# Kernel optimization log

Hardware: AMD Instinct MI355X
Metric: run time of the kernel (lower is better)

The kernel has to match this reference:

```python
import jax, jax.numpy as jnp
import numpy as np

HIDDEN = 1024
HEADS = 16
HEAD_DIM = HIDDEN // HEADS

def setup_inputs() -> dict:
    key = jax.random.key(0)
    k1, k2, k3 = jax.random.split(key, 3)
    scale = 1.0 / np.sqrt(HIDDEN)
    return {
        "x": jax.random.normal(k1, (2, 2048, HIDDEN), dtype=jnp.float32),
        "w_qkv": jax.random.normal(k2, (HIDDEN, 3 * HIDDEN), dtype=jnp.float32) * scale,
        "b_qkv": jnp.zeros((3 * HIDDEN,), dtype=jnp.float32),
        "w_out": jax.random.normal(k3, (HIDDEN, HIDDEN), dtype=jnp.float32) * scale,
        "b_out": jnp.zeros((HIDDEN,), dtype=jnp.float32),
    }

def reference(x, w_qkv, b_qkv, w_out, b_out):
    B, S, H = x.shape
    qkv = x @ w_qkv + b_qkv                              # (B,S,3H)
    qkv = qkv.reshape(B, S, 3, HEADS, HEAD_DIM)
    qkv = jnp.transpose(qkv, (2, 0, 3, 1, 4))            # (3,B,nh,S,hd)
    q, k, v = qkv[0], qkv[1], qkv[2]
    scores = jnp.einsum("bhqd,bhkd->bhqk", q, k) / np.sqrt(HEAD_DIM)
    causal = jnp.triu(jnp.ones((S, S), dtype=bool), k=1)  # True above diagonal
    scores = jnp.where(causal, -jnp.inf, scores)
    attn = jax.nn.softmax(scores, axis=-1)               # dropout: eval mode (identity)
    out = jnp.einsum("bhqk,bhkd->bhqd", attn, v)
    out = jnp.transpose(out, (0, 2, 1, 3)).reshape(B, S, H)
    return out @ w_out + b_out
```

## Files before the change

kernel.cpp:

```cpp
#include <hip/hip_runtime.h>
#include <hip/hip_bf16.h>

typedef short short8 __attribute__((ext_vector_type(8)));
typedef float f32x4 __attribute__((ext_vector_type(4)));

typedef const __attribute__((address_space(1))) unsigned int* gas_ptr;
typedef __attribute__((address_space(3))) unsigned int* las_ptr;
#define ASYNC16(g, l) __builtin_amdgcn_global_load_lds((gas_ptr)(g), (las_ptr)(l), 16, 0, 0)

__device__ __forceinline__ unsigned short f2bf(float f) {
    unsigned int u = __builtin_bit_cast(unsigned int, f);
    u += 0x7fff + ((u >> 16) & 1);
    return (unsigned short)(u >> 16);
}
__device__ __forceinline__ float bf2f(unsigned short s) {
    unsigned int u = (unsigned int)s << 16;
    return __builtin_bit_cast(float, u);
}
__device__ __forceinline__ unsigned int pkbf_trunc(float lo, float hi) {
    return __builtin_amdgcn_perm(__builtin_bit_cast(unsigned int, hi),
                                 __builtin_bit_cast(unsigned int, lo), 0x07060302u);
}
__device__ __forceinline__ float fexp2(float x) {
#if __has_builtin(__builtin_amdgcn_exp2f)
    return __builtin_amdgcn_exp2f(x);
#else
    return __expf(x * 0.6931471805599453f);
#endif
}

__device__ __forceinline__ void transpose_tile(
    const float* __restrict__ w, unsigned short* __restrict__ wt,
    int K, int N, int k0, int n0, unsigned short* tile)
{
    for (int i = threadIdx.x; i < 64 * 64; i += 256) {
        int r = i >> 6, c = i & 63;
        tile[r * 65 + c] = f2bf(w[(size_t)(k0 + r) * N + n0 + c]);
    }
    __syncthreads();
    for (int i = threadIdx.x; i < 64 * 64; i += 256) {
        int r = i >> 6, c = i & 63;
        wt[(size_t)(n0 + r) * K + k0 + c] = tile[c * 65 + r];
    }
}

__global__ __launch_bounds__(256) void prep(
    const float* __restrict__ x, const float* __restrict__ w_qkv,
    const float* __restrict__ w_out,
    unsigned short* __restrict__ x_b, unsigned short* __restrict__ wqkv_t,
    unsigned short* __restrict__ wout_t)
{
    __shared__ unsigned short tile[64 * 65];
    int bid = blockIdx.x;
    if (bid < 4096) {
        int i = (bid * 256 + threadIdx.x) * 4;
        float4 v = *(const float4*)(x + i);
        ushort4 o;
        o.x = f2bf(v.x); o.y = f2bf(v.y); o.z = f2bf(v.z); o.w = f2bf(v.w);
        *(ushort4*)(x_b + i) = o;
    } else if (bid < 4096 + 768) {
        int t = bid - 4096;
        transpose_tile(w_qkv, wqkv_t, 1024, 3072, (t / 48) * 64, (t % 48) * 64, tile);
    } else {
        int t = bid - 4864;
        transpose_tile(w_out, wout_t, 1024, 1024, (t >> 4) * 64, (t & 15) * 64, tile);
    }
}


template<bool OUT_BF16, bool QKV>
__global__ __launch_bounds__(256, 3) void gemm_bt(
    const unsigned short* __restrict__ A,
    const unsigned short* __restrict__ Bt,
    const float* __restrict__ bias,
    void* __restrict__ C,
    unsigned short* __restrict__ vTp,
    int M, int N, int K)
{
    __shared__ __align__(16) unsigned short As[2][128 * 32];
    __shared__ __align__(16) unsigned short Bs[2][128 * 32];
    const int tid = threadIdx.x;
    const int lane = tid & 63;
    const int wave = tid >> 6;
    const int wr = wave >> 1, wc = wave & 1;
    const int m0 = blockIdx.x * 128, n0 = blockIdx.y * 128;
    const int fr = lane & 15, fq = lane >> 4;

    f32x4 acc[4][4] = {};

    const int grow = lane >> 2;
    const int gcol = (lane & 3) * 8;
    const unsigned short* Ag = A  + (size_t)(m0 + wave * 32 + grow) * K + gcol;
    const unsigned short* Bg = Bt + (size_t)(n0 + wave * 32 + grow) * K + gcol;
    const int wb0 = (wave * 32) * 32;
    const int wb1 = (wave * 32 + 16) * 32;

    for (int k0 = 0; k0 < K; k0 += 64) {
        __syncthreads();
        ASYNC16(Ag + k0,               As[0] + wb0);
        ASYNC16(Ag + 16 * K + k0,      As[0] + wb1);
        ASYNC16(Bg + k0,               Bs[0] + wb0);
        ASYNC16(Bg + 16 * K + k0,      Bs[0] + wb1);
        ASYNC16(Ag + k0 + 32,          As[1] + wb0);
        ASYNC16(Ag + 16 * K + k0 + 32, As[1] + wb1);
        ASYNC16(Bg + k0 + 32,          Bs[1] + wb0);
        ASYNC16(Bg + 16 * K + k0 + 32, Bs[1] + wb1);
        __syncthreads();

#pragma unroll
        for (int h = 0; h < 2; h++) {
            short8 af[4], bfr[4];
#pragma unroll
            for (int i = 0; i < 4; i++)
                af[i] = *(const short8*)(As[h] + (wr * 64 + i * 16 + fr) * 32 + fq * 8);
#pragma unroll
            for (int j = 0; j < 4; j++)
                bfr[j] = *(const short8*)(Bs[h] + (wc * 64 + j * 16 + fr) * 32 + fq * 8);
#pragma unroll
            for (int i = 0; i < 4; i++)
#pragma unroll
                for (int j = 0; j < 4; j++)
                    acc[i][j] = __builtin_amdgcn_mfma_f32_16x16x32_bf16(af[i], bfr[j], acc[i][j], 0, 0, 0);
        }
    }

#pragma unroll
    for (int i = 0; i < 4; i++)
#pragma unroll
        for (int j = 0; j < 4; j++) {
            int col = n0 + wc * 64 + j * 16 + fr;
            float bv = bias[col];
            if (QKV && col >= 2048) {
                int hh = (col - 2048) >> 6, d = col & 63;
#pragma unroll
                for (int r = 0; r < 4; r++) {
                    int row = m0 + wr * 64 + i * 16 + fq * 4 + r;
                    int bb = row >> 11, s = row & 2047;
                    vTp[((size_t)(bb * 16 + hh) * 64 + d) * 2048 + s] = f2bf(acc[i][j][r] + bv);
                }
            } else {
                const int cstride = QKV ? 2048 : N;
#pragma unroll
                for (int r = 0; r < 4; r++) {
                    int row = m0 + wr * 64 + i * 16 + fq * 4 + r;
                    float v = acc[i][j][r] + bv;
                    if (OUT_BF16)
                        ((unsigned short*)C)[(size_t)row * cstride + col] = f2bf(v);
                    else
                        ((float*)C)[(size_t)row * cstride + col] = v;
                }
            }
        }
}


template<int RG0>
__device__ __forceinline__ void attn_step(
    const unsigned short* __restrict__ Ks0, const unsigned short* __restrict__ Ks1,
    const unsigned short* __restrict__ Vs0, const unsigned short* __restrict__ Vs1,
    unsigned short* __restrict__ Psw,
    const short8 (&qf)[4][2], const short8 ones,
    f32x4 (&o_acc)[4][4], f32x4 (&l_acc)[4],
    int j0, int fr, int fq,
    const int (&qrow0)[4], bool diagA, bool diagB)
{
    const int kpos = ((fq + (fr >> 1)) & 3) * 8;
    short8 kf[4][2];
#pragma unroll
    for (int t = 0; t < 4; t++) {
        kf[t][0] = *(const short8*)(Ks0 + (t * 16 + fr) * 32 + kpos);
        kf[t][1] = *(const short8*)(Ks1 + (t * 16 + fr) * 32 + kpos);
    }

    const float C1 = 0.18033688011112042f;
    const float C2 = -11.541560327111707f;

#pragma unroll
    for (int rg = RG0; rg < 4; rg++) {
        f32x4 s[4];
        __builtin_amdgcn_s_setprio(1);
#pragma unroll
        for (int t = 0; t < 4; t++) {
            s[t] = (f32x4){0.f, 0.f, 0.f, 0.f};
            s[t] = __builtin_amdgcn_mfma_f32_16x16x32_bf16(kf[t][0], qf[rg][0], s[t], 0, 0, 0);
            s[t] = __builtin_amdgcn_mfma_f32_16x16x32_bf16(kf[t][1], qf[rg][1], s[t], 0, 0, 0);
        }
        __builtin_amdgcn_s_setprio(0);
        const bool diag = (rg < 2) ? diagA : diagB;
        unsigned short* prow = Psw + rg * (16 * 64);
        const int qr = qrow0[rg] + fr;
        if (diag) {
#pragma unroll
            for (int t = 0; t < 4; t++) {
                const int kb = j0 + t * 16 + fq * 4;
                float p[4];
#pragma unroll
                for (int r = 0; r < 4; r++) {
                    float v = fexp2(s[t][r] * C1 + C2);
                    if (kb + r > qr) v = 0.f;
                    p[r] = v;
                }
                uint2 pk;
                pk.x = pkbf_trunc(p[0], p[1]);
                pk.y = pkbf_trunc(p[2], p[3]);
                const int blk = (t * 2 + (fq >> 1) + fr) & 7;
                *(uint2*)(prow + fr * 64 + blk * 8 + (fq & 1) * 4) = pk;
            }
        } else {
#pragma unroll
            for (int t = 0; t < 4; t++) {
                float p[4];
#pragma unroll
                for (int r = 0; r < 4; r++)
                    p[r] = fexp2(s[t][r] * C1 + C2);
                uint2 pk;
                pk.x = pkbf_trunc(p[0], p[1]);
                pk.y = pkbf_trunc(p[2], p[3]);
                const int blk = (t * 2 + (fq >> 1) + fr) & 7;
                *(uint2*)(prow + fr * 64 + blk * 8 + (fq & 1) * 4) = pk;
            }
        }
    }

#pragma unroll
    for (int ks = 0; ks < 2; ks++) {
        const unsigned short* Vsb = ks ? Vs1 : Vs0;
        const int colp = ((ks * 4 + fq + fr) & 7) * 8;
        short8 pf[4];
#pragma unroll
        for (int rg = RG0; rg < 4; rg++)
            pf[rg] = *(const short8*)(Psw + rg * (16 * 64) + fr * 64 + colp);
        __builtin_amdgcn_s_setprio(1);
#pragma unroll
        for (int t = 0; t < 4; t++) {
            short8 vf = *(const short8*)(Vsb + (t * 16 + fr) * 32 + kpos);
#pragma unroll
            for (int rg = RG0; rg < 4; rg++)
                o_acc[rg][t] = __builtin_amdgcn_mfma_f32_16x16x32_bf16(pf[rg], vf, o_acc[rg][t], 0, 0, 0);
        }
#pragma unroll
        for (int rg = RG0; rg < 4; rg++)
            l_acc[rg] = __builtin_amdgcn_mfma_f32_16x16x32_bf16(pf[rg], ones, l_acc[rg], 0, 0, 0);
        __builtin_amdgcn_s_setprio(0);
    }
}

__global__ __launch_bounds__(128, 2) void flash_attn(
    const unsigned short* __restrict__ qkv,
    const unsigned short* __restrict__ vT,
    unsigned short* __restrict__ Opart,
    float* __restrict__ lpart)
{
    const int p = blockIdx.x;
    const int g = blockIdx.y;
    const int h = blockIdx.z & 15, b = blockIdx.z >> 4;
    const int tid = threadIdx.x, wave = tid >> 6, lane = tid & 63;
    const int fr = lane & 15, fq = lane >> 4;
    const size_t RS = 2048;

    const unsigned short* Qb = qkv + (size_t)b * 2048 * RS + h * 64;
    const unsigned short* Kb = Qb + 1024;
    const unsigned short* Vt = vT + (size_t)(b * 16 + h) * 64 * 2048;

    __shared__ __align__(16) unsigned short Ks[2][64 * 32];
    __shared__ __align__(16) unsigned short Vs[2][64 * 32];
    __shared__ __align__(16) unsigned short Ps[2][4 * 16 * 64];

    short8 qf[4][2];
    int qrow0[4];
#pragma unroll
    for (int rg = 0; rg < 4; rg++) {
        int qt = (rg < 2) ? p : (31 - p);
        qrow0[rg] = qt * 64 + wave * 32 + (rg & 1) * 16;
        const unsigned short* qrow = Qb + (size_t)(qrow0[rg] + fr) * RS;
        qf[rg][0] = *(const short8*)(qrow + fq * 8);
        qf[rg][1] = *(const short8*)(qrow + 32 + fq * 8);
    }
    short8 ones;
#pragma unroll
    for (int e = 0; e < 8; e++) ones[e] = (short)0x3F80;

    f32x4 o_acc[4][4] = {};
    f32x4 l_acc[4] = {};

    const int grow = lane >> 2;
    const int gcol = (((lane & 3) - (grow >> 1)) & 3) * 8;
    const unsigned short* Kg = Kb + (size_t)(wave * 32 + grow) * RS + gcol;
    const unsigned short* Vg = Vt + (size_t)(wave * 32 + grow) * 2048 + gcol;
    const int wb = wave * 32 * 32;

    const int mid = (p >= 8) ? 8 : (16 - p);
    const int lo = g ? mid : 0;
    const int hi = g ? (32 - p) : mid;

    for (int jt = lo; jt < hi; jt++) {
        const int j0 = jt * 64;
        __syncthreads();
        ASYNC16(Kg + (size_t)j0 * RS,              Ks[0] + wb);
        ASYNC16(Kg + (size_t)(j0 + 16) * RS,       Ks[0] + wb + 512);
        ASYNC16(Kg + (size_t)j0 * RS + 32,         Ks[1] + wb);
        ASYNC16(Kg + (size_t)(j0 + 16) * RS + 32,  Ks[1] + wb + 512);
        ASYNC16(Vg + j0,                           Vs[0] + wb);
        ASYNC16(Vg + 16 * 2048 + j0,               Vs[0] + wb + 512);
        ASYNC16(Vg + j0 + 32,                      Vs[1] + wb);
        ASYNC16(Vg + 16 * 2048 + j0 + 32,          Vs[1] + wb + 512);
        __syncthreads();

        bool diagA = (jt == p), diagB = (jt == 31 - p);
        if (jt <= p)
            attn_step<0>(Ks[0], Ks[1], Vs[0], Vs[1], Ps[wave], qf, ones,
                         o_acc, l_acc, j0, fr, fq, qrow0, diagA, diagB);
        else
            attn_step<2>(Ks[0], Ks[1], Vs[0], Vs[1], Ps[wave], qf, ones,
                         o_acc, l_acc, j0, fr, fq, qrow0, diagA, diagB);
    }

    unsigned short* Og = Opart + (size_t)g * 4096 * 1024;
    float* lg = lpart + (size_t)g * 4096 * 16;
#pragma unroll
    for (int rg = 0; rg < 4; rg++) {
#pragma unroll
        for (int t = 0; t < 4; t++)
#pragma unroll
            for (int r = 0; r < 4; r++) {
                int row = qrow0[rg] + fq * 4 + r;
                Og[(size_t)(b * 2048 + row) * 1024 + h * 64 + t * 16 + fr] = f2bf(o_acc[rg][t][r]);
            }
        if (fr == 0) {
#pragma unroll
            for (int r = 0; r < 4; r++) {
                int row = qrow0[rg] + fq * 4 + r;
                lg[(size_t)(b * 2048 + row) * 16 + h] = l_acc[rg][r];
            }
        }
    }
}

__global__ __launch_bounds__(256) void reduce_attn(
    const unsigned short* __restrict__ Opart, const float* __restrict__ lpart,
    unsigned short* __restrict__ out)
{
    int i = (blockIdx.x * 256 + threadIdx.x) * 8;
    int row = i >> 10, h = (i & 1023) >> 6;
    float lsum = lpart[(size_t)row * 16 + h] + lpart[(size_t)4096 * 16 + row * 16 + h];
    float inv = 1.0f / lsum;
    ushort4 a0 = *(const ushort4*)(Opart + i);
    ushort4 a1 = *(const ushort4*)(Opart + i + 4);
    ushort4 b0 = *(const ushort4*)(Opart + (size_t)4096 * 1024 + i);
    ushort4 b1 = *(const ushort4*)(Opart + (size_t)4096 * 1024 + i + 4);
    ushort4 o0, o1;
    o0.x = f2bf((bf2f(a0.x) + bf2f(b0.x)) * inv);
    o0.y = f2bf((bf2f(a0.y) + bf2f(b0.y)) * inv);
    o0.z = f2bf((bf2f(a0.z) + bf2f(b0.z)) * inv);
    o0.w = f2bf((bf2f(a0.w) + bf2f(b0.w)) * inv);
    o1.x = f2bf((bf2f(a1.x) + bf2f(b1.x)) * inv);
    o1.y = f2bf((bf2f(a1.y) + bf2f(b1.y)) * inv);
    o1.z = f2bf((bf2f(a1.z) + bf2f(b1.z)) * inv);
    o1.w = f2bf((bf2f(a1.w) + bf2f(b1.w)) * inv);
    *(ushort4*)(out + i) = o0;
    *(ushort4*)(out + i + 4) = o1;
}

extern "C" void kernel_launch(void* const* d_in, const int* in_sizes, int n_in,
                              void* d_out, int out_size, void* d_ws, size_t ws_size,
                              hipStream_t stream) {
    const float* x      = (const float*)d_in[0];
    const float* w_qkv  = (const float*)d_in[1];
    const float* b_qkv  = (const float*)d_in[2];
    const float* w_out  = (const float*)d_in[3];
    const float* b_out  = (const float*)d_in[4];
    float* out = (float*)d_out;

    char* ws = (char*)d_ws;
    unsigned short* x_b    = (unsigned short*)(ws);
    unsigned short* wqkv_t = (unsigned short*)(ws + 8u  * 1024 * 1024);
    unsigned short* wout_t = (unsigned short*)(ws + 14u * 1024 * 1024);
    unsigned short* qkv    = (unsigned short*)(ws + 16u * 1024 * 1024);
    unsigned short* attn   = (unsigned short*)(ws + 32u * 1024 * 1024);
    unsigned short* vT     = (unsigned short*)(ws + 40u * 1024 * 1024);
    unsigned short* Opart  = (unsigned short*)(ws + 48u * 1024 * 1024);
    float*          lpart  = (float*)         (ws + 64u * 1024 * 1024);

    prep<<<5120, 256, 0, stream>>>(x, w_qkv, w_out, x_b, wqkv_t, wout_t);
    gemm_bt<true, true ><<<dim3(32, 24), 256, 0, stream>>>(x_b,  wqkv_t, b_qkv, qkv, vT, 4096, 3072, 1024);
    flash_attn<<<dim3(16, 2, 32), 128, 0, stream>>>(qkv, vT, Opart, lpart);
    reduce_attn<<<2048, 256, 0, stream>>>(Opart, lpart, attn);
    gemm_bt<false, false><<<dim3(32, 8),  256, 0, stream>>>(attn, wout_t, b_out, out, nullptr, 4096, 1024, 1024);
}
```

Baseline: 187.3 us.

## Split attention KV range four ways with 32-key tiles and four-way reduction

Shrinks the flash-attention key tile from 64 to 32 keys, which halves the LDS footprint for K, V and P, and splits each block's key range into four partitions of balanced work instead of two. The grid doubles to 4 partitions and the reduce kernel now sums four partial O and l buffers. The goal is more blocks in flight and better load balance across CUs. The cost is twice as many barriers per key, twice the partial-output traffic, and a heavier reduction pass.

```diff
diff --git a/kernel.cpp b/kernel.cpp
--- a/kernel.cpp
+++ b/kernel.cpp
@@ -157,7 +157,7 @@
 template<int RG0>
 __device__ __forceinline__ void attn_step(
     const unsigned short* __restrict__ Ks0, const unsigned short* __restrict__ Ks1,
-    const unsigned short* __restrict__ Vs0, const unsigned short* __restrict__ Vs1,
+    const unsigned short* __restrict__ Vsb,
     unsigned short* __restrict__ Psw,
     const short8 (&qf)[4][2], const short8 ones,
     f32x4 (&o_acc)[4][4], f32x4 (&l_acc)[4],
@@ -165,9 +165,9 @@
     const int (&qrow0)[4], bool diagA, bool diagB)
 {
     const int kpos = ((fq + (fr >> 1)) & 3) * 8;
-    short8 kf[4][2];
-#pragma unroll
-    for (int t = 0; t < 4; t++) {
+    short8 kf[2][2];
+#pragma unroll
+    for (int t = 0; t < 2; t++) {
         kf[t][0] = *(const short8*)(Ks0 + (t * 16 + fr) * 32 + kpos);
         kf[t][1] = *(const short8*)(Ks1 + (t * 16 + fr) * 32 + kpos);
     }
@@ -177,21 +177,21 @@
 
 #pragma unroll
     for (int rg = RG0; rg < 4; rg++) {
-        f32x4 s[4];
+        f32x4 s[2];
         __builtin_amdgcn_s_setprio(1);
 #pragma unroll
-        for (int t = 0; t < 4; t++) {
+        for (int t = 0; t < 2; t++) {
             s[t] = (f32x4){0.f, 0.f, 0.f, 0.f};
             s[t] = __builtin_amdgcn_mfma_f32_16x16x32_bf16(kf[t][0], qf[rg][0], s[t], 0, 0, 0);
             s[t] = __builtin_amdgcn_mfma_f32_16x16x32_bf16(kf[t][1], qf[rg][1], s[t], 0, 0, 0);
         }
         __builtin_amdgcn_s_setprio(0);
         const bool diag = (rg < 2) ? diagA : diagB;
-        unsigned short* prow = Psw + rg * (16 * 64);
+        unsigned short* prow = Psw + rg * (16 * 32);
         const int qr = qrow0[rg] + fr;
         if (diag) {
 #pragma unroll
-            for (int t = 0; t < 4; t++) {
+            for (int t = 0; t < 2; t++) {
                 const int kb = j0 + t * 16 + fq * 4;
                 float p[4];
 #pragma unroll
@@ -203,12 +203,12 @@
                 uint2 pk;
                 pk.x = pkbf_trunc(p[0], p[1]);
                 pk.y = pkbf_trunc(p[2], p[3]);
-                const int blk = (t * 2 + (fq >> 1) + fr) & 7;
-                *(uint2*)(prow + fr * 64 + blk * 8 + (fq & 1) * 4) = pk;
+                const int blk = (t * 2 + (fq >> 1) + (fr >> 1)) & 3;
+                *(uint2*)(prow + fr * 32 + blk * 8 + (fq & 1) * 4) = pk;
             }
         } else {
 #pragma unroll
-            for (int t = 0; t < 4; t++) {
+            for (int t = 0; t < 2; t++) {
                 float p[4];
 #pragma unroll
                 for (int r = 0; r < 4; r++)
@@ -216,20 +216,17 @@
                 uint2 pk;
                 pk.x = pkbf_trunc(p[0], p[1]);
                 pk.y = pkbf_trunc(p[2], p[3]);
-                const int blk = (t * 2 + (fq >> 1) + fr) & 7;
-                *(uint2*)(prow + fr * 64 + blk * 8 + (fq & 1) * 4) = pk;
-            }
-        }
-    }
-
-#pragma unroll
-    for (int ks = 0; ks < 2; ks++) {
-        const unsigned short* Vsb = ks ? Vs1 : Vs0;
-        const int colp = ((ks * 4 + fq + fr) & 7) * 8;
+                const int blk = (t * 2 + (fq >> 1) + (fr >> 1)) & 3;
+                *(uint2*)(prow + fr * 32 + blk * 8 + (fq & 1) * 4) = pk;
+            }
+        }
+    }
+
+    {
         short8 pf[4];
 #pragma unroll
         for (int rg = RG0; rg < 4; rg++)
-            pf[rg] = *(const short8*)(Psw + rg * (16 * 64) + fr * 64 + colp);
+            pf[rg] = *(const short8*)(Psw + rg * (16 * 32) + fr * 32 + kpos);
         __builtin_amdgcn_s_setprio(1);
 #pragma unroll
         for (int t = 0; t < 4; t++) {
@@ -262,9 +259,9 @@
     const unsigned short* Kb = Qb + 1024;
     const unsigned short* Vt = vT + (size_t)(b * 16 + h) * 64 * 2048;
 
-    __shared__ __align__(16) unsigned short Ks[2][64 * 32];
-    __shared__ __align__(16) unsigned short Vs[2][64 * 32];
-    __shared__ __align__(16) unsigned short Ps[2][4 * 16 * 64];
+    __shared__ __align__(16) unsigned short Ks[2][32 * 32];
+    __shared__ __align__(16) unsigned short Vs[64 * 32];
+    __shared__ __align__(16) unsigned short Ps[2][4 * 16 * 32];
 
     short8 qf[4][2];
     int qrow0[4];
@@ -284,35 +281,31 @@
     f32x4 l_acc[4] = {};
 
     const int grow = lane >> 2;
-    const int gcol = (((lane & 3) - (grow >> 1)) & 3) * 8;
-    const unsigned short* Kg = Kb + (size_t)(wave * 32 + grow) * RS + gcol;
-    const unsigned short* Vg = Vt + (size_t)(wave * 32 + grow) * 2048 + gcol;
-    const int wb = wave * 32 * 32;
-
-    const int mid = (p >= 8) ? 8 : (16 - p);
-    const int lo = g ? mid : 0;
-    const int hi = g ? (32 - p) : mid;
+    const int gswz = (((lane & 3) - (grow >> 1)) & 3) * 8;
+    const unsigned short* KgR = Kb + (size_t)(wave * 16 + grow) * RS + gswz;
+    const unsigned short* VgR = Vt + (size_t)(wave * 32 + grow) * 2048 + gswz;
+
+    const int c8 = 8 * p + 8;
+    const int T0 = g * 33, T1 = T0 + 33;
+    const int lo = (T0 <= c8) ? ((T0 + 2) >> 2) : (2 * p + 2 + ((T0 - c8 + 1) >> 1));
+    const int hi = (T1 <= c8) ? ((T1 + 2) >> 2) : (2 * p + 2 + ((T1 - c8 + 1) >> 1));
 
     for (int jt = lo; jt < hi; jt++) {
-        const int j0 = jt * 64;
+        const int j0 = jt * 32;
         __syncthreads();
-        ASYNC16(Kg + (size_t)j0 * RS,              Ks[0] + wb);
-        ASYNC16(Kg + (size_t)(j0 + 16) * RS,       Ks[0] + wb + 512);
-        ASYNC16(Kg + (size_t)j0 * RS + 32,         Ks[1] + wb);
-        ASYNC16(Kg + (size_t)(j0 + 16) * RS + 32,  Ks[1] + wb + 512);
-        ASYNC16(Vg + j0,                           Vs[0] + wb);
-        ASYNC16(Vg + 16 * 2048 + j0,               Vs[0] + wb + 512);
-        ASYNC16(Vg + j0 + 32,                      Vs[1] + wb);
-        ASYNC16(Vg + 16 * 2048 + j0 + 32,          Vs[1] + wb + 512);
+        ASYNC16(KgR + (size_t)j0 * RS,       Ks[0] + wave * 512);
+        ASYNC16(KgR + (size_t)j0 * RS + 32,  Ks[1] + wave * 512);
+        ASYNC16(VgR + j0,                    Vs + wave * 1024);
+        ASYNC16(VgR + 16 * 2048 + j0,        Vs + wave * 1024 + 512);
         __syncthreads();
 
-        bool diagA = (jt == p), diagB = (jt == 31 - p);
-        if (jt <= p)
-            attn_step<0>(Ks[0], Ks[1], Vs[0], Vs[1], Ps[wave], qf, ones,
-                         o_acc, l_acc, j0, fr, fq, qrow0, diagA, diagB);
+        const bool dA = ((jt >> 1) == p), dB = ((jt >> 1) == 31 - p);
+        if ((jt >> 1) <= p)
+            attn_step<0>(Ks[0], Ks[1], Vs, Ps[wave], qf, ones,
+                         o_acc, l_acc, j0, fr, fq, qrow0, dA, dB);
         else
-            attn_step<2>(Ks[0], Ks[1], Vs[0], Vs[1], Ps[wave], qf, ones,
-                         o_acc, l_acc, j0, fr, fq, qrow0, diagA, diagB);
+            attn_step<2>(Ks[0], Ks[1], Vs, Ps[wave], qf, ones,
+                         o_acc, l_acc, j0, fr, fq, qrow0, dA, dB);
     }
 
     unsigned short* Og = Opart + (size_t)g * 4096 * 1024;
@@ -342,21 +335,25 @@
 {
     int i = (blockIdx.x * 256 + threadIdx.x) * 8;
     int row = i >> 10, h = (i & 1023) >> 6;
-    float lsum = lpart[(size_t)row * 16 + h] + lpart[(size_t)4096 * 16 + row * 16 + h];
+    float lsum = 0.f;
+#pragma unroll
+    for (int g = 0; g < 4; g++)
+        lsum += lpart[(size_t)g * 4096 * 16 + row * 16 + h];
     float inv = 1.0f / lsum;
-    ushort4 a0 = *(const ushort4*)(Opart + i);
-    ushort4 a1 = *(const ushort4*)(Opart + i + 4);
-    ushort4 b0 = *(const ushort4*)(Opart + (size_t)4096 * 1024 + i);
-    ushort4 b1 = *(const ushort4*)(Opart + (size_t)4096 * 1024 + i + 4);
+    float acc[8] = {0.f, 0.f, 0.f, 0.f, 0.f, 0.f, 0.f, 0.f};
+#pragma unroll
+    for (int g = 0; g < 4; g++) {
+        const unsigned short* Op = Opart + (size_t)g * 4096 * 1024 + i;
+        ushort4 a0 = *(const ushort4*)(Op);
+        ushort4 a1 = *(const ushort4*)(Op + 4);
+        acc[0] += bf2f(a0.x); acc[1] += bf2f(a0.y); acc[2] += bf2f(a0.z); acc[3] += bf2f(a0.w);
+        acc[4] += bf2f(a1.x); acc[5] += bf2f(a1.y); acc[6] += bf2f(a1.z); acc[7] += bf2f(a1.w);
+    }
     ushort4 o0, o1;
-    o0.x = f2bf((bf2f(a0.x) + bf2f(b0.x)) * inv);
-    o0.y = f2bf((bf2f(a0.y) + bf2f(b0.y)) * inv);
-    o0.z = f2bf((bf2f(a0.z) + bf2f(b0.z)) * inv);
-    o0.w = f2bf((bf2f(a0.w) + bf2f(b0.w)) * inv);
-    o1.x = f2bf((bf2f(a1.x) + bf2f(b1.x)) * inv);
-    o1.y = f2bf((bf2f(a1.y) + bf2f(b1.y)) * inv);
-    o1.z = f2bf((bf2f(a1.z) + bf2f(b1.z)) * inv);
-    o1.w = f2bf((bf2f(a1.w) + bf2f(b1.w)) * inv);
+    o0.x = f2bf(acc[0] * inv); o0.y = f2bf(acc[1] * inv);
+    o0.z = f2bf(acc[2] * inv); o0.w = f2bf(acc[3] * inv);
+    o1.x = f2bf(acc[4] * inv); o1.y = f2bf(acc[5] * inv);
+    o1.z = f2bf(acc[6] * inv); o1.w = f2bf(acc[7] * inv);
     *(ushort4*)(out + i) = o0;
     *(ushort4*)(out + i + 4) = o1;
 }
@@ -379,11 +376,11 @@
     unsigned short* attn   = (unsigned short*)(ws + 32u * 1024 * 1024);
     unsigned short* vT     = (unsigned short*)(ws + 40u * 1024 * 1024);
     unsigned short* Opart  = (unsigned short*)(ws + 48u * 1024 * 1024);
-    float*          lpart  = (float*)         (ws + 64u * 1024 * 1024);
+    float*          lpart  = (float*)         (ws + 80u * 1024 * 1024);
 
     prep<<<5120, 256, 0, stream>>>(x, w_qkv, w_out, x_b, wqkv_t, wout_t);
     gemm_bt<true, true ><<<dim3(32, 24), 256, 0, stream>>>(x_b,  wqkv_t, b_qkv, qkv, vT, 4096, 3072, 1024);
-    flash_attn<<<dim3(16, 2, 32), 128, 0, stream>>>(qkv, vT, Opart, lpart);
+    flash_attn<<<dim3(16, 4, 32), 128, 0, stream>>>(qkv, vT, Opart, lpart);
     reduce_attn<<<2048, 256, 0, stream>>>(Opart, lpart, attn);
     gemm_bt<false, false><<<dim3(32, 8),  256, 0, stream>>>(attn, wout_t, b_out, out, nullptr, 4096, 1024, 1024);
 }
```

After: 201.9 us. 7.8% more time.
